# Kernel optimization log

Hardware: AMD Instinct MI355X
Metric: run time of the kernel (lower is better)

The kernel has to match this reference:

```python
import jax, jax.numpy as jnp
import numpy as np

HEADS = 8
DIM_HEAD = 64
DIM = 512
HIDDEN = HEADS * DIM_HEAD  # 512


def setup_inputs() -> dict:
    key = jax.random.key(0)
    k1, k2, k3, k4 = jax.random.split(key, 4)
    B, H, W = 8, 64, 64
    x = jax.random.normal(k1, (B, DIM, H, W), dtype=jnp.float32)
    # Conv2d 1x1 weights stored as [out_ch, in_ch] (kernel 1x1 squeezed)
    w_qkv = jax.random.normal(k2, (3 * HIDDEN, DIM), dtype=jnp.float32) * (1.0 / np.sqrt(DIM))
    w_out = jax.random.normal(k3, (DIM, HIDDEN), dtype=jnp.float32) * (1.0 / np.sqrt(HIDDEN))
    b_out = jax.random.normal(k4, (DIM,), dtype=jnp.float32) * 0.01
    return {"x": x, "w_qkv": w_qkv, "w_out": w_out, "b_out": b_out}


def reference(x, w_qkv, w_out, b_out):
    b, c, h, w = x.shape
    n = h * w
    # to_qkv: 1x1 conv == channel GEMM
    qkv = jnp.einsum('bchw,oc->bohw', x, w_qkv)               # [b, 3*heads*dh, h, w]
    qkv = qkv.reshape(b, 3, HEADS, DIM_HEAD, n)               # split (qkv heads c), flatten (h w)
    q, k, v = qkv[:, 0], qkv[:, 1], qkv[:, 2]                 # each [b, heads, dh, n]
    k = jax.nn.softmax(k, axis=-1)                            # softmax over spatial tokens
    context = jnp.einsum('bhdn,bhen->bhde', k, v)             # [b, heads, dh, dh]
    out = jnp.einsum('bhde,bhdn->bhen', context, q)           # [b, heads, dh, n]
    out = out.reshape(b, HIDDEN, h, w)
    # to_out: 1x1 conv with bias
    return jnp.einsum('bchw,oc->bohw', out, w_out) + b_out[None, :, None, None]
```

## Files before the change

### kernel.cpp

```cpp
#include <hip/hip_runtime.h>
#include <hip/hip_bf16.h>


typedef __attribute__((ext_vector_type(8))) __bf16 bf16x8;
typedef __attribute__((ext_vector_type(4))) float f32x4;
typedef __attribute__((ext_vector_type(8))) unsigned short u16x8;

__device__ __forceinline__ unsigned short f2b(float f) {
  unsigned int u = __builtin_bit_cast(unsigned int, f);
  unsigned int r = (u + 0x7FFFu + ((u >> 16) & 1u)) >> 16;
  return (unsigned short)r;
}
__device__ __forceinline__ float b2f(unsigned short h) {
  unsigned int u = ((unsigned int)h) << 16;
  return __builtin_bit_cast(float, u);
}

__global__ __launch_bounds__(256) void wconv_kernel(const float* __restrict__ w,
                                                    unsigned short* __restrict__ wb) {
  int i = (blockIdx.x * 256 + threadIdx.x) * 4;
  #pragma unroll
  for (int j = 0; j < 4; ++j) wb[i + j] = f2b(w[i + j]);
}

__global__ __launch_bounds__(256) void transpose_x_kernel(const float* __restrict__ x,
                                                          unsigned short* __restrict__ xT) {
  __shared__ unsigned short tile[64][65];
  const int b = blockIdx.z, ct = blockIdx.y, nt = blockIdx.x;
  const int c0 = ct * 64, n0 = nt * 64;
  const int tc = threadIdx.x & 63, tr = threadIdx.x >> 6;
  const float* xp = x + ((long)b * 512 + c0) * 4096 + n0;
  #pragma unroll
  for (int i = 0; i < 16; ++i) {
    int row = tr * 16 + i;
    tile[tc][row] = f2b(xp[(long)row * 4096 + tc]);
  }
  __syncthreads();
  unsigned short* xtp = xT + ((long)b * 4096 + n0) * 512 + c0;
  #pragma unroll
  for (int i = 0; i < 16; ++i) {
    int row = tr * 16 + i;
    xtp[(long)row * 512 + tc] = tile[row][tc];
  }
}

__global__ __launch_bounds__(256) void transpose_q_kernel(const unsigned short* __restrict__ qkv,
                                                          unsigned short* __restrict__ qT) {
  __shared__ unsigned short tile[64][65];
  const int b = blockIdx.z, et = blockIdx.y, nt = blockIdx.x;
  const int e0 = et * 64, n0 = nt * 64;
  const int tc = threadIdx.x & 63, tr = threadIdx.x >> 6;
  const unsigned short* qp = qkv + ((long)b * 1536 + e0) * 4096 + n0;
  #pragma unroll
  for (int i = 0; i < 16; ++i) {
    int row = tr * 16 + i;
    tile[tc][row] = qp[(long)row * 4096 + tc];
  }
  __syncthreads();
  unsigned short* qtp = qT + ((long)b * 4096 + n0) * 512 + e0;
  #pragma unroll
  for (int i = 0; i < 16; ++i) {
    int row = tr * 16 + i;
    qtp[(long)row * 512 + tc] = tile[row][tc];
  }
}

__global__ __launch_bounds__(256) void gemm128_bt(
    const unsigned short* __restrict__ A, long strideA,
    const unsigned short* __restrict__ BT, long strideBT,
    void* __restrict__ Cout, long strideC,
    const float* __restrict__ bias) {
  constexpr int K = 512;
  constexpr int N = 4096;
  const int b = blockIdx.z;
  const int m0 = blockIdx.y * 128;
  const int n0 = blockIdx.x * 128;
  const unsigned short* Ab = A + (long)b * strideA;
  const unsigned short* Bb = BT + (long)b * strideBT;

  __shared__ unsigned short lds[2 * 128 * 64];
  char* ldsc = (char*)lds;

  const int tid = threadIdx.x;
  const int wave = tid >> 6;
  const int lane = tid & 63;
  const int wr = wave >> 1;
  const int wc = wave & 1;

  f32x4 acc[4][4];
  const f32x4 zero = {0.f, 0.f, 0.f, 0.f};
  #pragma unroll
  for (int i = 0; i < 4; ++i)
    #pragma unroll
    for (int j = 0; j < 4; ++j) acc[i][j] = zero;

  for (int kt = 0; kt < K; kt += 64) {
    #pragma unroll
    for (int q = 0; q < 4; ++q) {
      unsigned base = q * 4096 + wave * 1024;
      unsigned D = base + lane * 16;
      unsigned row = D >> 7;
      unsigned g = (D >> 4) & 7;
      unsigned gl = g ^ (row & 7);
      const unsigned short* srcA = Ab + (long)(m0 + row) * K + kt + gl * 8;
      __builtin_amdgcn_global_load_lds(
          (const __attribute__((address_space(1))) unsigned int*)srcA,
          (__attribute__((address_space(3))) unsigned int*)(ldsc + base), 16, 0, 0);
      const unsigned short* srcB = Bb + (long)(n0 + row) * K + kt + gl * 8;
      __builtin_amdgcn_global_load_lds(
          (const __attribute__((address_space(1))) unsigned int*)srcB,
          (__attribute__((address_space(3))) unsigned int*)(ldsc + 16384 + base), 16, 0, 0);
    }
    __syncthreads();

    bf16x8 af[2][4], bfr[2][4];
    #pragma unroll
    for (int ks = 0; ks < 2; ++ks) {
      #pragma unroll
      for (int mi = 0; mi < 4; ++mi) {
        unsigned row = wr * 64 + mi * 16 + (lane & 15);
        unsigned g = ((unsigned)(ks * 4 + (lane >> 4))) ^ (row & 7);
        af[ks][mi] = *(const bf16x8*)(ldsc + row * 128 + g * 16);
      }
      #pragma unroll
      for (int ni = 0; ni < 4; ++ni) {
        unsigned row = wc * 64 + ni * 16 + (lane & 15);
        unsigned g = ((unsigned)(ks * 4 + (lane >> 4))) ^ (row & 7);
        bfr[ks][ni] = *(const bf16x8*)(ldsc + 16384 + row * 128 + g * 16);
      }
    }
    #pragma unroll
    for (int ks = 0; ks < 2; ++ks)
      #pragma unroll
      for (int mi = 0; mi < 4; ++mi)
        #pragma unroll
        for (int ni = 0; ni < 4; ++ni)
          acc[mi][ni] = __builtin_amdgcn_mfma_f32_16x16x32_bf16(
              af[ks][mi], bfr[ks][ni], acc[mi][ni], 0, 0, 0);
    __syncthreads();
  }

  const int r0 = (lane >> 4) * 4;
  const int cn = lane & 15;
  if (bias != nullptr) {
    float* C = (float*)Cout + (long)b * strideC;
    #pragma unroll
    for (int mi = 0; mi < 4; ++mi) {
      int o = m0 + wr * 64 + mi * 16 + r0;
      #pragma unroll
      for (int ni = 0; ni < 4; ++ni) {
        int n = n0 + wc * 64 + ni * 16 + cn;
        #pragma unroll
        for (int r = 0; r < 4; ++r)
          C[(long)(o + r) * N + n] = acc[mi][ni][r] + bias[o + r];
      }
    }
  } else {
    unsigned short* C = (unsigned short*)Cout + (long)b * strideC;
    #pragma unroll
    for (int mi = 0; mi < 4; ++mi) {
      int o = m0 + wr * 64 + mi * 16 + r0;
      #pragma unroll
      for (int ni = 0; ni < 4; ++ni) {
        int n = n0 + wc * 64 + ni * 16 + cn;
        #pragma unroll
        for (int r = 0; r < 4; ++r)
          C[(long)(o + r) * N + n] = f2b(acc[mi][ni][r]);
      }
    }
  }
}

__global__ __launch_bounds__(256) void softmax_k_kernel(unsigned short* __restrict__ qkv) {
  const int row = blockIdx.x;
  const int b = row >> 9, d = row & 511;
  unsigned short* kp = qkv + ((long)b * 1536 + 512 + d) * 4096;
  const int tid = threadIdx.x, wave = tid >> 6, lane = tid & 63;
  __shared__ float red[8];

  float v[16];
  u16x8 l0 = *(const u16x8*)(kp + tid * 8);
  u16x8 l1 = *(const u16x8*)(kp + 2048 + tid * 8);
  #pragma unroll
  for (int j = 0; j < 8; ++j) { v[j] = b2f(l0[j]); v[8 + j] = b2f(l1[j]); }

  float m = v[0];
  #pragma unroll
  for (int j = 1; j < 16; ++j) m = fmaxf(m, v[j]);
  #pragma unroll
  for (int off = 32; off > 0; off >>= 1) m = fmaxf(m, __shfl_xor(m, off));
  if (lane == 0) red[wave] = m;
  __syncthreads();
  m = fmaxf(fmaxf(red[0], red[1]), fmaxf(red[2], red[3]));

  float s = 0.f;
  #pragma unroll
  for (int j = 0; j < 16; ++j) { v[j] = __expf(v[j] - m); s += v[j]; }
  #pragma unroll
  for (int off = 32; off > 0; off >>= 1) s += __shfl_xor(s, off);
  if (lane == 0) red[4 + wave] = s;
  __syncthreads();
  s = red[4] + red[5] + red[6] + red[7];
  float inv = 1.0f / s;

  u16x8 o0, o1;
  #pragma unroll
  for (int j = 0; j < 8; ++j) { o0[j] = f2b(v[j] * inv); o1[j] = f2b(v[8 + j] * inv); }
  *(u16x8*)(kp + tid * 8) = o0;
  *(u16x8*)(kp + 2048 + tid * 8) = o1;
}

__global__ __launch_bounds__(256) void context_kernel(const unsigned short* __restrict__ qkv,
                                                      float* __restrict__ ctx) {
  const int bh = blockIdx.x, b = bh >> 3, h = bh & 7;
  const unsigned short* Kp = qkv + ((long)b * 1536 + 512 + h * 64) * 4096;
  const unsigned short* Vp = qkv + ((long)b * 1536 + 1024 + h * 64) * 4096;
  const int tid = threadIdx.x, wave = tid >> 6, lane = tid & 63;

  f32x4 acc[4][4];
  const f32x4 zero = {0.f, 0.f, 0.f, 0.f};
  #pragma unroll
  for (int i = 0; i < 4; ++i)
    #pragma unroll
    for (int j = 0; j < 4; ++j) acc[i][j] = zero;

  const int kbeg = wave * 1024;
  for (int k0 = kbeg; k0 < kbeg + 1024; k0 += 32) {
    const int kc = k0 + (lane >> 4) * 8;
    bf16x8 a[4], bv[4];
    #pragma unroll
    for (int mi = 0; mi < 4; ++mi)
      a[mi] = *(const bf16x8*)(Kp + (long)(mi * 16 + (lane & 15)) * 4096 + kc);
    #pragma unroll
    for (int ni = 0; ni < 4; ++ni)
      bv[ni] = *(const bf16x8*)(Vp + (long)(ni * 16 + (lane & 15)) * 4096 + kc);
    #pragma unroll
    for (int mi = 0; mi < 4; ++mi)
      #pragma unroll
      for (int ni = 0; ni < 4; ++ni)
        acc[mi][ni] = __builtin_amdgcn_mfma_f32_16x16x32_bf16(a[mi], bv[ni], acc[mi][ni], 0, 0, 0);
  }

  __shared__ float part[4][64][64];
  #pragma unroll
  for (int mi = 0; mi < 4; ++mi)
    #pragma unroll
    for (int ni = 0; ni < 4; ++ni)
      #pragma unroll
      for (int r = 0; r < 4; ++r)
        part[wave][mi * 16 + (lane >> 4) * 4 + r][ni * 16 + (lane & 15)] = acc[mi][ni][r];
  __syncthreads();
  float* cp = ctx + (long)bh * 4096;
  for (int i = tid; i < 4096; i += 256) {
    int dd = i >> 6, ee = i & 63;
    cp[i] = part[0][dd][ee] + part[1][dd][ee] + part[2][dd][ee] + part[3][dd][ee];
  }
}

__global__ __launch_bounds__(256) void w2_kernel(const float* __restrict__ ctx,
                                                 const float* __restrict__ w_out,
                                                 unsigned short* __restrict__ W2) {
  const int cc = blockIdx.x, bh = blockIdx.y, b = bh >> 3, h = bh & 7;
  __shared__ float cs[64][65];
  const int tid = threadIdx.x;
  for (int i = tid; i < 4096; i += 256) cs[i >> 6][i & 63] = ctx[(long)bh * 4096 + i];
  __syncthreads();
  const int c = cc * 64 + (tid >> 2);
  const int d0 = (tid & 3) * 16;
  float wrow[64];
  const float* wp = w_out + (long)c * 512 + h * 64;
  #pragma unroll
  for (int e = 0; e < 64; ++e) wrow[e] = wp[e];
  unsigned short* W2p = W2 + ((long)b * 512 + c) * 512 + h * 64;
  #pragma unroll 4
  for (int dd = 0; dd < 16; ++dd) {
    float s = 0.f;
    #pragma unroll
    for (int e = 0; e < 64; ++e) s = fmaf(wrow[e], cs[d0 + dd][e], s);
    W2p[d0 + dd] = f2b(s);
  }
}

extern "C" void kernel_launch(void* const* d_in, const int* in_sizes, int n_in,
                              void* d_out, int out_size, void* d_ws, size_t ws_size,
                              hipStream_t stream) {
  const float* x     = (const float*)d_in[0];
  const float* w_qkv = (const float*)d_in[1];
  const float* w_out = (const float*)d_in[2];
  const float* b_out = (const float*)d_in[3];

  char* ws = (char*)d_ws;
  unsigned short* qkv = (unsigned short*)ws;
  unsigned short* xT  = (unsigned short*)(ws + 100663296);
  unsigned short* qT  = xT;
  unsigned short* wqb = (unsigned short*)(ws + 134217728);
  float*          ctx = (float*)(ws + 135790592);
  unsigned short* W2  = (unsigned short*)(ws + 136839168);

  wconv_kernel<<<dim3(768), dim3(256), 0, stream>>>(w_qkv, wqb);
  transpose_x_kernel<<<dim3(64, 8, 8), dim3(256), 0, stream>>>(x, xT);
  gemm128_bt<<<dim3(32, 12, 8), dim3(256), 0, stream>>>(
      wqb, 0L, xT, (long)4096 * 512, (void*)qkv, (long)1536 * 4096, (const float*)nullptr);
  softmax_k_kernel<<<dim3(4096), dim3(256), 0, stream>>>(qkv);
  transpose_q_kernel<<<dim3(64, 8, 8), dim3(256), 0, stream>>>(qkv, qT);
  context_kernel<<<dim3(64), dim3(256), 0, stream>>>(qkv, ctx);
  w2_kernel<<<dim3(8, 64), dim3(256), 0, stream>>>(ctx, w_out, W2);
  gemm128_bt<<<dim3(32, 4, 8), dim3(256), 0, stream>>>(
      W2, (long)512 * 512, qT, (long)4096 * 512, d_out, (long)512 * 4096, b_out);
}
```

Before: 194.0 us.

## Fold Wq into output weights, fuse softmax into context, split context over N

Q is no longer materialised. The per-batch matrix W2·Wq is precomputed as W3 with a small GEMM, and the final GEMM multiplies it directly with the transposed x. This removes the Q third of the QKV GEMM and the Q transpose. Softmax is reduced to a row-stats kernel storing max and inverse sum, with the exponentiation done on the fly inside the context kernel. The context kernel is now split 8 ways along N to use more CUs, with the partial sums reduced in w2_kernel. The cost is that exp is recomputed in the context kernel and an extra small GEMM launch is added.

```diff
diff --git a/kernel.cpp b/kernel.cpp
--- a/kernel.cpp
+++ b/kernel.cpp
@@ -16,11 +16,31 @@
   return __builtin_bit_cast(float, u);
 }
 
-__global__ __launch_bounds__(256) void wconv_kernel(const float* __restrict__ w,
-                                                    unsigned short* __restrict__ wb) {
+__global__ __launch_bounds__(256) void prep_wkv_kernel(const float* __restrict__ w,
+                                                       unsigned short* __restrict__ wkv) {
   int i = (blockIdx.x * 256 + threadIdx.x) * 4;
-  #pragma unroll
-  for (int j = 0; j < 4; ++j) wb[i + j] = f2b(w[i + j]);
+  const float* src = w + 512 * 512;
+  #pragma unroll
+  for (int j = 0; j < 4; ++j) wkv[i + j] = f2b(src[i + j]);
+}
+
+__global__ __launch_bounds__(256) void prep_wqT_kernel(const float* __restrict__ w,
+                                                       unsigned short* __restrict__ WqT) {
+  __shared__ unsigned short tile[64][65];
+  const int ct = blockIdx.x, ot = blockIdx.y;
+  const int c0 = ct * 64, o0 = ot * 64;
+  const int tc = threadIdx.x & 63, tr = threadIdx.x >> 6;
+  #pragma unroll
+  for (int i = 0; i < 16; ++i) {
+    int row = tr * 16 + i;
+    tile[tc][row] = f2b(w[(long)(o0 + row) * 512 + c0 + tc]);
+  }
+  __syncthreads();
+  #pragma unroll
+  for (int i = 0; i < 16; ++i) {
+    int row = tr * 16 + i;
+    WqT[(long)(c0 + row) * 512 + o0 + tc] = tile[row][tc];
+  }
 }
 
 __global__ __launch_bounds__(256) void transpose_x_kernel(const float* __restrict__ x,
@@ -44,34 +64,12 @@
   }
 }
 
-__global__ __launch_bounds__(256) void transpose_q_kernel(const unsigned short* __restrict__ qkv,
-                                                          unsigned short* __restrict__ qT) {
-  __shared__ unsigned short tile[64][65];
-  const int b = blockIdx.z, et = blockIdx.y, nt = blockIdx.x;
-  const int e0 = et * 64, n0 = nt * 64;
-  const int tc = threadIdx.x & 63, tr = threadIdx.x >> 6;
-  const unsigned short* qp = qkv + ((long)b * 1536 + e0) * 4096 + n0;
-  #pragma unroll
-  for (int i = 0; i < 16; ++i) {
-    int row = tr * 16 + i;
-    tile[tc][row] = qp[(long)row * 4096 + tc];
-  }
-  __syncthreads();
-  unsigned short* qtp = qT + ((long)b * 4096 + n0) * 512 + e0;
-  #pragma unroll
-  for (int i = 0; i < 16; ++i) {
-    int row = tr * 16 + i;
-    qtp[(long)row * 512 + tc] = tile[row][tc];
-  }
-}
-
 __global__ __launch_bounds__(256) void gemm128_bt(
     const unsigned short* __restrict__ A, long strideA,
     const unsigned short* __restrict__ BT, long strideBT,
-    void* __restrict__ Cout, long strideC,
+    void* __restrict__ Cout, long strideC, int ldc,
     const float* __restrict__ bias) {
   constexpr int K = 512;
-  constexpr int N = 4096;
   const int b = blockIdx.z;
   const int m0 = blockIdx.y * 128;
   const int n0 = blockIdx.x * 128;
@@ -152,7 +150,7 @@
         int n = n0 + wc * 64 + ni * 16 + cn;
         #pragma unroll
         for (int r = 0; r < 4; ++r)
-          C[(long)(o + r) * N + n] = acc[mi][ni][r] + bias[o + r];
+          C[(long)(o + r) * ldc + n] = acc[mi][ni][r] + bias[o + r];
       }
     }
   } else {
@@ -165,16 +163,17 @@
         int n = n0 + wc * 64 + ni * 16 + cn;
         #pragma unroll
         for (int r = 0; r < 4; ++r)
-          C[(long)(o + r) * N + n] = f2b(acc[mi][ni][r]);
+          C[(long)(o + r) * ldc + n] = f2b(acc[mi][ni][r]);
       }
     }
   }
 }
 
-__global__ __launch_bounds__(256) void softmax_k_kernel(unsigned short* __restrict__ qkv) {
+__global__ __launch_bounds__(256) void rowstat_kernel(const unsigned short* __restrict__ kv,
+                                                      float* __restrict__ stats) {
   const int row = blockIdx.x;
   const int b = row >> 9, d = row & 511;
-  unsigned short* kp = qkv + ((long)b * 1536 + 512 + d) * 4096;
+  const unsigned short* kp = kv + ((long)b * 1024 + d) * 4096;
   const int tid = threadIdx.x, wave = tid >> 6, lane = tid & 63;
   __shared__ float red[8];
 
@@ -195,27 +194,34 @@
 
   float s = 0.f;
   #pragma unroll
-  for (int j = 0; j < 16; ++j) { v[j] = __expf(v[j] - m); s += v[j]; }
+  for (int j = 0; j < 16; ++j) s += __expf(v[j] - m);
   #pragma unroll
   for (int off = 32; off > 0; off >>= 1) s += __shfl_xor(s, off);
   if (lane == 0) red[4 + wave] = s;
   __syncthreads();
-  s = red[4] + red[5] + red[6] + red[7];
-  float inv = 1.0f / s;
-
-  u16x8 o0, o1;
-  #pragma unroll
-  for (int j = 0; j < 8; ++j) { o0[j] = f2b(v[j] * inv); o1[j] = f2b(v[8 + j] * inv); }
-  *(u16x8*)(kp + tid * 8) = o0;
-  *(u16x8*)(kp + 2048 + tid * 8) = o1;
-}
-
-__global__ __launch_bounds__(256) void context_kernel(const unsigned short* __restrict__ qkv,
-                                                      float* __restrict__ ctx) {
-  const int bh = blockIdx.x, b = bh >> 3, h = bh & 7;
-  const unsigned short* Kp = qkv + ((long)b * 1536 + 512 + h * 64) * 4096;
-  const unsigned short* Vp = qkv + ((long)b * 1536 + 1024 + h * 64) * 4096;
+  if (tid == 0) {
+    s = red[4] + red[5] + red[6] + red[7];
+    stats[2 * row] = m;
+    stats[2 * row + 1] = 1.0f / s;
+  }
+}
+
+__global__ __launch_bounds__(256) void context_kernel(const unsigned short* __restrict__ kv,
+                                                      const float* __restrict__ stats,
+                                                      float* __restrict__ ctx_part) {
+  const int s = blockIdx.x, bh = blockIdx.y, b = bh >> 3, h = bh & 7;
+  const unsigned short* Kp = kv + ((long)b * 1024 + h * 64) * 4096;
+  const unsigned short* Vp = kv + ((long)b * 1024 + 512 + h * 64) * 4096;
+  const float* sb = stats + ((long)b * 512 + h * 64) * 2;
   const int tid = threadIdx.x, wave = tid >> 6, lane = tid & 63;
+
+  float mrow[4], srow[4];
+  #pragma unroll
+  for (int mi = 0; mi < 4; ++mi) {
+    int rA = mi * 16 + (lane & 15);
+    mrow[mi] = sb[2 * rA];
+    srow[mi] = sb[2 * rA + 1];
+  }
 
   f32x4 acc[4][4];
   const f32x4 zero = {0.f, 0.f, 0.f, 0.f};
@@ -224,13 +230,19 @@
     #pragma unroll
     for (int j = 0; j < 4; ++j) acc[i][j] = zero;
 
-  const int kbeg = wave * 1024;
-  for (int k0 = kbeg; k0 < kbeg + 1024; k0 += 32) {
+  const int kbeg = s * 512 + wave * 128;
+  for (int k0 = kbeg; k0 < kbeg + 128; k0 += 32) {
     const int kc = k0 + (lane >> 4) * 8;
     bf16x8 a[4], bv[4];
     #pragma unroll
-    for (int mi = 0; mi < 4; ++mi)
-      a[mi] = *(const bf16x8*)(Kp + (long)(mi * 16 + (lane & 15)) * 4096 + kc);
+    for (int mi = 0; mi < 4; ++mi) {
+      u16x8 kr = *(const u16x8*)(Kp + (long)(mi * 16 + (lane & 15)) * 4096 + kc);
+      u16x8 pr;
+      #pragma unroll
+      for (int j = 0; j < 8; ++j)
+        pr[j] = f2b(__expf(b2f(kr[j]) - mrow[mi]) * srow[mi]);
+      a[mi] = __builtin_bit_cast(bf16x8, pr);
+    }
     #pragma unroll
     for (int ni = 0; ni < 4; ++ni)
       bv[ni] = *(const bf16x8*)(Vp + (long)(ni * 16 + (lane & 15)) * 4096 + kc);
@@ -250,34 +262,38 @@
       for (int r = 0; r < 4; ++r)
         part[wave][mi * 16 + (lane >> 4) * 4 + r][ni * 16 + (lane & 15)] = acc[mi][ni][r];
   __syncthreads();
-  float* cp = ctx + (long)bh * 4096;
+  float* cp = ctx_part + ((long)(s * 64 + bh)) * 4096;
   for (int i = tid; i < 4096; i += 256) {
     int dd = i >> 6, ee = i & 63;
     cp[i] = part[0][dd][ee] + part[1][dd][ee] + part[2][dd][ee] + part[3][dd][ee];
   }
 }
 
-__global__ __launch_bounds__(256) void w2_kernel(const float* __restrict__ ctx,
+__global__ __launch_bounds__(256) void w2_kernel(const float* __restrict__ ctx_part,
                                                  const float* __restrict__ w_out,
                                                  unsigned short* __restrict__ W2) {
-  const int cc = blockIdx.x, bh = blockIdx.y, b = bh >> 3, h = bh & 7;
+  const int cq = blockIdx.x, bh = blockIdx.y, b = bh >> 3, h = bh & 7;
   __shared__ float cs[64][65];
   const int tid = threadIdx.x;
-  for (int i = tid; i < 4096; i += 256) cs[i >> 6][i & 63] = ctx[(long)bh * 4096 + i];
-  __syncthreads();
-  const int c = cc * 64 + (tid >> 2);
-  const int d0 = (tid & 3) * 16;
+  for (int i = tid; i < 4096; i += 256) {
+    float v = 0.f;
+    #pragma unroll
+    for (int s = 0; s < 8; ++s) v += ctx_part[((long)(s * 64 + bh)) * 4096 + i];
+    cs[i >> 6][i & 63] = v;
+  }
+  __syncthreads();
+  const int c = cq * 128 + (tid & 127);
+  const int dbeg = (tid >> 7) * 32;
+  const float* wp = w_out + (long)c * 512 + h * 64;
   float wrow[64];
-  const float* wp = w_out + (long)c * 512 + h * 64;
   #pragma unroll
   for (int e = 0; e < 64; ++e) wrow[e] = wp[e];
   unsigned short* W2p = W2 + ((long)b * 512 + c) * 512 + h * 64;
-  #pragma unroll 4
-  for (int dd = 0; dd < 16; ++dd) {
+  for (int dd = dbeg; dd < dbeg + 32; ++dd) {
     float s = 0.f;
     #pragma unroll
-    for (int e = 0; e < 64; ++e) s = fmaf(wrow[e], cs[d0 + dd][e], s);
-    W2p[d0 + dd] = f2b(s);
+    for (int e = 0; e < 64; ++e) s = fmaf(wrow[e], cs[dd][e], s);
+    W2p[dd] = f2b(s);
   }
 }
 
@@ -290,21 +306,25 @@
   const float* b_out = (const float*)d_in[3];
 
   char* ws = (char*)d_ws;
-  unsigned short* qkv = (unsigned short*)ws;
-  unsigned short* xT  = (unsigned short*)(ws + 100663296);
-  unsigned short* qT  = xT;
-  unsigned short* wqb = (unsigned short*)(ws + 134217728);
-  float*          ctx = (float*)(ws + 135790592);
-  unsigned short* W2  = (unsigned short*)(ws + 136839168);
-
-  wconv_kernel<<<dim3(768), dim3(256), 0, stream>>>(w_qkv, wqb);
+  unsigned short* xT   = (unsigned short*)ws;
+  unsigned short* kv   = (unsigned short*)(ws + 33554432);
+  unsigned short* wkv  = (unsigned short*)(ws + 100663296);
+  unsigned short* WqT  = (unsigned short*)(ws + 101711872);
+  float*          stats= (float*)(ws + 102236160);
+  float*          ctxp = (float*)(ws + 102268928);
+  unsigned short* W2   = (unsigned short*)(ws + 110657536);
+  unsigned short* W3   = (unsigned short*)(ws + 114851840);
+
+  prep_wkv_kernel<<<dim3(512), dim3(256), 0, stream>>>(w_qkv, wkv);
+  prep_wqT_kernel<<<dim3(8, 8), dim3(256), 0, stream>>>(w_qkv, WqT);
   transpose_x_kernel<<<dim3(64, 8, 8), dim3(256), 0, stream>>>(x, xT);
-  gemm128_bt<<<dim3(32, 12, 8), dim3(256), 0, stream>>>(
-      wqb, 0L, xT, (long)4096 * 512, (void*)qkv, (long)1536 * 4096, (const float*)nullptr);
-  softmax_k_kernel<<<dim3(4096), dim3(256), 0, stream>>>(qkv);
-  transpose_q_kernel<<<dim3(64, 8, 8), dim3(256), 0, stream>>>(qkv, qT);
-  context_kernel<<<dim3(64), dim3(256), 0, stream>>>(qkv, ctx);
-  w2_kernel<<<dim3(8, 64), dim3(256), 0, stream>>>(ctx, w_out, W2);
+  gemm128_bt<<<dim3(32, 8, 8), dim3(256), 0, stream>>>(
+      wkv, 0L, xT, (long)4096 * 512, (void*)kv, (long)1024 * 4096, 4096, (const float*)nullptr);
+  rowstat_kernel<<<dim3(4096), dim3(256), 0, stream>>>(kv, stats);
+  context_kernel<<<dim3(8, 64), dim3(256), 0, stream>>>(kv, stats, ctxp);
+  w2_kernel<<<dim3(4, 64), dim3(256), 0, stream>>>(ctxp, w_out, W2);
+  gemm128_bt<<<dim3(4, 4, 8), dim3(256), 0, stream>>>(
+      W2, (long)512 * 512, WqT, 0L, (void*)W3, (long)512 * 512, 512, (const float*)nullptr);
   gemm128_bt<<<dim3(32, 4, 8), dim3(256), 0, stream>>>(
-      W2, (long)512 * 512, qT, (long)4096 * 512, d_out, (long)512 * 4096, b_out);
-}
+      W3, (long)512 * 512, xT, (long)4096 * 512, d_out, (long)512 * 4096, 4096, b_out);
+}
```

Result: faster. 166.3 us (-14.3%).
